# Kernel tuning notes

Hardware: AMD Instinct MI355X
Metric: run time of the kernel (lower is better)

The kernel has to match this reference:

```python
import jax, jax.numpy as jnp
import numpy as np

BITS = 8192      # num_neurons / output bits per step
NB_T = 10        # n_bits_per_neuron for transition RAM (min(bits+4,10))
NB_I = 4         # n_bits_per_neuron for initial RAM
POS = 4          # position encoding bits
LENGTH = 4096


def setup_inputs() -> dict:
    key = jax.random.key(0)
    k1, k2, k3, k4 = jax.random.split(key, 4)
    # RAM contents are binary (0/1) stored as float32 for the kernel baseline
    transition_memory = (jax.random.uniform(k1, (BITS, 2 ** NB_T)) > 0.5).astype(jnp.float32)
    initial_memory = (jax.random.uniform(k2, (BITS, 2 ** NB_I)) > 0.5).astype(jnp.float32)
    # each neuron taps NB random bit positions of its input
    transition_connections = jax.random.randint(k3, (BITS, NB_T), 0, BITS + POS, dtype=jnp.int32)
    initial_connections = jax.random.randint(k4, (BITS, NB_I), 0, POS, dtype=jnp.int32)
    return {
        "transition_memory": transition_memory,
        "initial_memory": initial_memory,
        "transition_connections": transition_connections,
        "initial_connections": initial_connections,
        "length": LENGTH,
    }


def _pos_bits(pos):
    # matches _encode_pos: bits[3] = LSB, bits[0] = MSB of low 4 bits
    return ((pos >> jnp.arange(3, -1, -1, dtype=jnp.int32)) & 1).astype(jnp.int32)


def _ram(x_bits, connections, memory):
    # x_bits: [total_input_bits] int32 in {0,1}
    sel = x_bits[connections]                                  # [N, n]
    n = connections.shape[1]
    pw = (2 ** jnp.arange(n - 1, -1, -1)).astype(jnp.int32)    # bit -> address weight
    addr = (sel * pw).sum(-1)                                  # [N]
    return jnp.take_along_axis(memory, addr[:, None], axis=1)[:, 0]  # [N]


def reference(transition_memory, initial_memory, transition_connections, initial_connections, length):
    # step 0: initial RAM addressed by position bits only
    out0 = _ram(_pos_bits(jnp.int32(0)), initial_connections, initial_memory)  # [BITS] float {0,1}

    def step(prev_bits, i):
        inp = jnp.concatenate([prev_bits, _pos_bits(i)])                      # [BITS+4]
        out = _ram(inp, transition_connections, transition_memory)            # [BITS]
        return (out > 0.5).astype(jnp.int32), out

    _, outs = jax.lax.scan(step, (out0 > 0.5).astype(jnp.int32),
                           jnp.arange(1, length, dtype=jnp.int32))
    return jnp.concatenate([out0[None, :], outs], axis=0)  # [length, BITS]
```

## Files before the change

kernel.cpp:

```cpp
#include <hip/hip_runtime.h>
#include <stdint.h>


#define BITS   8192
#define NBT    10
#define NBLK   32
#define TPB    256
#define NPB    (BITS / NBLK)
#define SWORDS 256
#define WPB    (NPB / 32)
#define TWORDS (NPB * 32)
#define FUSE   (1 << 12)

__global__ void pack_kernel(const float* __restrict__ tm, uint32_t* __restrict__ packed) {
    int tid = blockIdx.x * blockDim.x + threadIdx.x;
    float v = tm[tid];
    unsigned long long m = __ballot(v > 0.5f);
    int lane = tid & 63;
    if ((lane & 31) == 0) {
        packed[tid >> 5] = (lane == 0) ? (uint32_t)m : (uint32_t)(m >> 32);
    }
}

__global__ __launch_bounds__(TPB) void ram_step_kernel(
    const int* __restrict__ conn,
    const float* __restrict__ init_mem,
    const uint32_t* __restrict__ packedT,
    unsigned long long* __restrict__ pairs,
    float* __restrict__ out,
    int length)
{
    const int b = blockIdx.x;
    const int t = threadIdx.x;
    const int lane = t & 63;
    const int n = b * NPB + t;

    __shared__ uint32_t st[2][SWORDS + 1];
    __shared__ uint32_t tbl[TWORDS];

    {
        const uint32_t* tp = packedT + (size_t)b * TWORDS;
#pragma unroll
        for (int k = 0; k < 8; ++k) {
            int w = k * 1024 + t * 4;
            uint4 v = *(const uint4*)(tp + w);
            *(uint4*)&tbl[w] = v;
        }
    }

    int c[NBT];
#pragma unroll
    for (int j = 0; j < NBT; ++j) c[j] = conn[n * NBT + j];

    const int gw = b * WPB + (t >> 6) * 2;

    float v0 = init_mem[n << 4];
    int bit = (v0 > 0.5f) ? 1 : 0;
    unsigned long long m = __ballot(bit);
    if (lane == 0) {
        const unsigned long long tag = 1ull << 32;
        __hip_atomic_store(&pairs[gw],     tag | (uint32_t)m,
                           __ATOMIC_RELAXED, __HIP_MEMORY_SCOPE_AGENT);
        __hip_atomic_store(&pairs[gw + 1], tag | (uint32_t)(m >> 32),
                           __ATOMIC_RELAXED, __HIP_MEMORY_SCOPE_AGENT);
        st[0][gw]     = (uint32_t)m;
        st[0][gw + 1] = (uint32_t)(m >> 32);
    }
    out[n] = v0;

    for (int i = 1; i < length; ++i) {
        uint32_t* sb = st[(i - 1) & 1];
        const uint32_t want = (uint32_t)i;

        if (t == 0) {
            sb[SWORDS] = ((i >> 3) & 1) | (((i >> 2) & 1) << 1) |
                         (((i >> 1) & 1) << 2) | ((i & 1) << 3);
        }
        if ((t >> 3) != b) {
            unsigned long long* p = &pairs[((i - 1) & 1) * SWORDS + t];
            unsigned long long pv;
            int fuse = 0;
            do {
                pv = __hip_atomic_load(p, __ATOMIC_RELAXED, __HIP_MEMORY_SCOPE_AGENT);
            } while ((uint32_t)(pv >> 32) != want && ++fuse < FUSE);
            sb[t] = (uint32_t)pv;
        }
        __syncthreads();

        uint32_t addr = 0;
#pragma unroll
        for (int j = 0; j < NBT; ++j) {
            int cc = c[j];
            addr = (addr << 1) | ((sb[cc >> 5] >> (cc & 31)) & 1u);
        }
        uint32_t pw = tbl[(t << 5) + (addr >> 5)];
        bit = (pw >> (addr & 31)) & 1;

        m = __ballot(bit);
        if (lane == 0) {
            const unsigned long long tag = ((unsigned long long)(i + 1)) << 32;
            const int base = (i & 1) * SWORDS + gw;
            __hip_atomic_store(&pairs[base],     tag | (uint32_t)m,
                               __ATOMIC_RELAXED, __HIP_MEMORY_SCOPE_AGENT);
            __hip_atomic_store(&pairs[base + 1], tag | (uint32_t)(m >> 32),
                               __ATOMIC_RELAXED, __HIP_MEMORY_SCOPE_AGENT);
            st[i & 1][gw]     = (uint32_t)m;
            st[i & 1][gw + 1] = (uint32_t)(m >> 32);
        }
        out[(size_t)i * BITS + n] = (float)bit;
    }
}

extern "C" void kernel_launch(void* const* d_in, const int* in_sizes, int n_in,
                              void* d_out, int out_size, void* d_ws, size_t ws_size,
                              hipStream_t stream) {
    const float* tm = (const float*)d_in[0];
    const float* im = (const float*)d_in[1];
    const int*   tc = (const int*)d_in[2];
    const int length = out_size / BITS;

    uint32_t* packed = (uint32_t*)d_ws;
    unsigned long long* pairs =
        (unsigned long long*)((char*)d_ws + (1 << 20));

    hipMemsetAsync(pairs, 0, 2 * SWORDS * sizeof(unsigned long long), stream);

    pack_kernel<<<dim3((BITS * 1024) / 256), dim3(256), 0, stream>>>(tm, packed);

    ram_step_kernel<<<dim3(NBLK), dim3(TPB), 0, stream>>>(
        tc, im, packed, pairs, (float*)d_out, length);
}
```

Baseline: 6.202 ms.

## Form single-XCD team of blocks and poll L2-scoped flags for step exchange

Launches an oversized grid, reads each block's XCC ID, and elects the first XCD that gathers 16 blocks to run the recurrence. Each block now covers twice as many neurons with 512 threads, and the other blocks exit. Because all team blocks share one L2, step bits are published and polled with sc0 (L2-coherent) loads and stores instead of agent-scope atomics, which should cut inter-block latency per step. A fallback to agent-scope polling handles timeouts, at the cost of extra complexity, an inline-asm dependency and a longer team-formation phase.

```diff
diff --git a/kernel.cpp b/kernel.cpp
--- a/kernel.cpp
+++ b/kernel.cpp
@@ -4,13 +4,16 @@
 
 #define BITS   8192
 #define NBT    10
-#define NBLK   32
-#define TPB    256
-#define NPB    (BITS / NBLK)
+#define NTEAM  16
+#define TPB    512
+#define NPB    (BITS / NTEAM)
 #define SWORDS 256
 #define WPB    (NPB / 32)
 #define TWORDS (NPB * 32)
-#define FUSE   (1 << 12)
+#define GRID   256
+#define SE_FUSE   256
+#define AG_FUSE   (1 << 14)
+#define FORM_FUSE (1 << 20)
 
 __global__ void pack_kernel(const float* __restrict__ tm, uint32_t* __restrict__ packed) {
     int tid = blockIdx.x * blockDim.x + threadIdx.x;
@@ -22,18 +25,61 @@
     }
 }
 
+__device__ __forceinline__ uint64_t poll_se(const uint64_t* p) {
+    uint64_t v;
+    asm volatile("global_load_dwordx2 %0, %1, off sc0\n\t"
+                 "s_waitcnt vmcnt(0)"
+                 : "=v"(v) : "v"(p) : "memory");
+    return v;
+}
+__device__ __forceinline__ void pub_se(uint64_t* p, uint64_t v) {
+    asm volatile("global_store_dwordx2 %0, %1, off sc0"
+                 : : "v"(p), "v"(v) : "memory");
+}
+
 __global__ __launch_bounds__(TPB) void ram_step_kernel(
     const int* __restrict__ conn,
     const float* __restrict__ init_mem,
     const uint32_t* __restrict__ packedT,
-    unsigned long long* __restrict__ pairs,
+    uint64_t* __restrict__ pairs_ag,
+    uint64_t* __restrict__ pairs_se,
+    int* __restrict__ claim,
     float* __restrict__ out,
     int length)
 {
-    const int b = blockIdx.x;
+    int xcc;
+    asm volatile("s_getreg_b32 %0, hwreg(HW_REG_XCC_ID)" : "=s"(xcc));
+    xcc &= 0xF;
+
+    __shared__ int s_slot;
+    __shared__ int s_bad;
     const int t = threadIdx.x;
-    const int lane = t & 63;
-    const int n = b * NPB + t;
+    if (t == 0) {
+        s_bad = 0;
+        int slot = -1;
+        int mine = __hip_atomic_fetch_add(&claim[xcc], 1,
+                        __ATOMIC_RELAXED, __HIP_MEMORY_SCOPE_AGENT);
+        if (mine == NTEAM - 1) {
+            int expected = 0;
+            __hip_atomic_compare_exchange_strong(&claim[16], &expected,
+                        xcc | 0x100, __ATOMIC_RELAXED, __ATOMIC_RELAXED,
+                        __HIP_MEMORY_SCOPE_AGENT);
+        }
+        int lead = 0, fuse = 0;
+        do {
+            lead = __hip_atomic_load(&claim[16],
+                        __ATOMIC_RELAXED, __HIP_MEMORY_SCOPE_AGENT);
+        } while (lead == 0 && ++fuse < FORM_FUSE);
+        if (lead != 0 && (lead & 0xFF) == xcc) {
+            int s = __hip_atomic_fetch_add(&claim[17], 1,
+                        __ATOMIC_RELAXED, __HIP_MEMORY_SCOPE_AGENT);
+            if (s < NTEAM) slot = s;
+        }
+        s_slot = slot;
+    }
+    __syncthreads();
+    const int b = s_slot;
+    if (b < 0) return;
 
     __shared__ uint32_t st[2][SWORDS + 1];
     __shared__ uint32_t tbl[TWORDS];
@@ -42,26 +88,31 @@
         const uint32_t* tp = packedT + (size_t)b * TWORDS;
 #pragma unroll
         for (int k = 0; k < 8; ++k) {
-            int w = k * 1024 + t * 4;
-            uint4 v = *(const uint4*)(tp + w);
-            *(uint4*)&tbl[w] = v;
+            int w = (k * TPB + t) * 4;
+            *(uint4*)&tbl[w] = *(const uint4*)(tp + w);
         }
     }
 
     int c[NBT];
 #pragma unroll
-    for (int j = 0; j < NBT; ++j) c[j] = conn[n * NBT + j];
-
+    for (int j = 0; j < NBT; ++j) c[j] = conn[(b * NPB + t) * NBT + j];
+
+    const int lane = t & 63;
+    const int n = b * NPB + t;
     const int gw = b * WPB + (t >> 6) * 2;
+    bool fast = true;
 
     float v0 = init_mem[n << 4];
     int bit = (v0 > 0.5f) ? 1 : 0;
     unsigned long long m = __ballot(bit);
     if (lane == 0) {
-        const unsigned long long tag = 1ull << 32;
-        __hip_atomic_store(&pairs[gw],     tag | (uint32_t)m,
+        const uint64_t tag = 1ull << 32;
+        uint64_t w0 = tag | (uint32_t)m, w1 = tag | (uint32_t)(m >> 32);
+        pub_se(&pairs_se[gw], w0);
+        pub_se(&pairs_se[gw + 1], w1);
+        __hip_atomic_store(&pairs_ag[gw], w0,
                            __ATOMIC_RELAXED, __HIP_MEMORY_SCOPE_AGENT);
-        __hip_atomic_store(&pairs[gw + 1], tag | (uint32_t)(m >> 32),
+        __hip_atomic_store(&pairs_ag[gw + 1], w1,
                            __ATOMIC_RELAXED, __HIP_MEMORY_SCOPE_AGENT);
         st[0][gw]     = (uint32_t)m;
         st[0][gw + 1] = (uint32_t)(m >> 32);
@@ -71,21 +122,35 @@
     for (int i = 1; i < length; ++i) {
         uint32_t* sb = st[(i - 1) & 1];
         const uint32_t want = (uint32_t)i;
+        const int par = (i - 1) & 1;
 
         if (t == 0) {
             sb[SWORDS] = ((i >> 3) & 1) | (((i >> 2) & 1) << 1) |
                          (((i >> 1) & 1) << 2) | ((i & 1) << 3);
         }
-        if ((t >> 3) != b) {
-            unsigned long long* p = &pairs[((i - 1) & 1) * SWORDS + t];
-            unsigned long long pv;
-            int fuse = 0;
-            do {
-                pv = __hip_atomic_load(p, __ATOMIC_RELAXED, __HIP_MEMORY_SCOPE_AGENT);
-            } while ((uint32_t)(pv >> 32) != want && ++fuse < FUSE);
+        if (t < SWORDS && (t >> 4) != b) {
+            uint64_t pv = 0;
+            bool ok = false;
+            if (fast) {
+                const uint64_t* p = &pairs_se[par * SWORDS + t];
+                for (int f = 0; f < SE_FUSE; ++f) {
+                    pv = poll_se(p);
+                    if ((uint32_t)(pv >> 32) == want) { ok = true; break; }
+                }
+                if (!ok) s_bad = 1;
+            }
+            if (!ok) {
+                const uint64_t* p = &pairs_ag[par * SWORDS + t];
+                int f = 0;
+                do {
+                    pv = __hip_atomic_load(p, __ATOMIC_RELAXED,
+                                           __HIP_MEMORY_SCOPE_AGENT);
+                } while ((uint32_t)(pv >> 32) != want && ++f < AG_FUSE);
+            }
             sb[t] = (uint32_t)pv;
         }
         __syncthreads();
+        if (s_bad) fast = false;
 
         uint32_t addr = 0;
 #pragma unroll
@@ -98,11 +163,16 @@
 
         m = __ballot(bit);
         if (lane == 0) {
-            const unsigned long long tag = ((unsigned long long)(i + 1)) << 32;
+            const uint64_t tag = ((uint64_t)(i + 1)) << 32;
             const int base = (i & 1) * SWORDS + gw;
-            __hip_atomic_store(&pairs[base],     tag | (uint32_t)m,
+            uint64_t w0 = tag | (uint32_t)m, w1 = tag | (uint32_t)(m >> 32);
+            if (fast) {
+                pub_se(&pairs_se[base], w0);
+                pub_se(&pairs_se[base + 1], w1);
+            }
+            __hip_atomic_store(&pairs_ag[base], w0,
                                __ATOMIC_RELAXED, __HIP_MEMORY_SCOPE_AGENT);
-            __hip_atomic_store(&pairs[base + 1], tag | (uint32_t)(m >> 32),
+            __hip_atomic_store(&pairs_ag[base + 1], w1,
                                __ATOMIC_RELAXED, __HIP_MEMORY_SCOPE_AGENT);
             st[i & 1][gw]     = (uint32_t)m;
             st[i & 1][gw + 1] = (uint32_t)(m >> 32);
@@ -119,14 +189,15 @@
     const int*   tc = (const int*)d_in[2];
     const int length = out_size / BITS;
 
-    uint32_t* packed = (uint32_t*)d_ws;
-    unsigned long long* pairs =
-        (unsigned long long*)((char*)d_ws + (1 << 20));
-
-    hipMemsetAsync(pairs, 0, 2 * SWORDS * sizeof(unsigned long long), stream);
+    uint32_t* packed   = (uint32_t*)d_ws;
+    uint64_t* pairs_ag = (uint64_t*)((char*)d_ws + (1 << 20));
+    uint64_t* pairs_se = (uint64_t*)((char*)d_ws + (1 << 20) + 4096);
+    int*      claim    = (int*)((char*)d_ws + (1 << 20) + 8192);
+
+    hipMemsetAsync((char*)d_ws + (1 << 20), 0, 8192 + 128, stream);
 
     pack_kernel<<<dim3((BITS * 1024) / 256), dim3(256), 0, stream>>>(tm, packed);
 
-    ram_step_kernel<<<dim3(NBLK), dim3(TPB), 0, stream>>>(
-        tc, im, packed, pairs, (float*)d_out, length);
-}
+    ram_step_kernel<<<dim3(GRID), dim3(TPB), 0, stream>>>(
+        tc, im, packed, pairs_ag, pairs_se, claim, (float*)d_out, length);
+}
```

Result: slower. 10.95 ms (+76.6%).
